# Kernel tuning notes

Hardware: AMD Instinct MI355X
Metric: run time of the kernel (lower is better)

## Reference

```python
import jax, jax.numpy as jnp
import numpy as np

HIDDEN = 1024


def setup_inputs() -> dict:
    key = jax.random.key(0)
    ks = jax.random.split(key, 8)
    x_in, y_in, out_dim, hidden = 1024, 1024, 1024, HIDDEN
    Nx, Ny = 4096, 4096
    s = lambda d: 1.0 / np.sqrt(d)
    return {
        "x": jax.random.normal(ks[0], (Nx, x_in), jnp.float32),
        "y": jax.random.normal(ks[1], (Ny, y_in), jnp.float32),
        "Wq": jax.random.normal(ks[2], (hidden, x_in), jnp.float32) * s(x_in),
        "bq": jnp.zeros((hidden,), jnp.float32),
        "Wk": jax.random.normal(ks[3], (hidden, y_in), jnp.float32) * s(y_in),
        "bk": jnp.zeros((hidden,), jnp.float32),
        "Wv": jax.random.normal(ks[4], (out_dim, y_in), jnp.float32) * s(y_in),
        "bv": jnp.zeros((out_dim,), jnp.float32),
    }


def reference(x, y, Wq, bq, Wk, bk, Wv, bv):
    # Linear projections (torch Linear: x @ W.T + b)
    q = x @ Wq.T + bq          # [Nx, H]
    k = y @ Wk.T + bk          # [Ny, H]
    v = y @ Wv.T + bv          # [Ny, D_out]
    scores = (q @ k.T) / jnp.sqrt(jnp.asarray(HIDDEN, q.dtype))  # [Nx, Ny]
    attn = jax.nn.softmax(scores, axis=1)
    return attn @ v            # [Nx, D_out]
```

## Files before the change

kernel.cpp:

```cpp
#include <hip/hip_runtime.h>
#include <cstdint>
#include <cstddef>

typedef __attribute__((ext_vector_type(8))) __bf16 bf16x8;
typedef __attribute__((ext_vector_type(4))) float  f32x4;

__device__ __forceinline__ unsigned short f32_to_bf16(float f) {
    union { float f; unsigned int u; } cv;
    cv.f = f;
    unsigned int u = cv.u;
    return (unsigned short)((u + 0x7fffu + ((u >> 16) & 1u)) >> 16);
}

__device__ __forceinline__ float bf16_to_f32(unsigned short h) {
    union { unsigned int u; float f; } cv;
    cv.u = ((unsigned int)h) << 16;
    return cv.f;
}

__device__ __forceinline__ void async_copy16(const unsigned short* g, unsigned short* lds) {
    __builtin_amdgcn_global_load_lds(
        (const __attribute__((address_space(1))) unsigned int*)g,
        (__attribute__((address_space(3))) unsigned int*)lds,
        16, 0, 0);
}

__global__ __launch_bounds__(256) void cast_all(
    const float* __restrict__ x,  const float* __restrict__ y,
    const float* __restrict__ wq, const float* __restrict__ wk, const float* __restrict__ wv,
    unsigned short* __restrict__ xb,  unsigned short* __restrict__ yb,
    unsigned short* __restrict__ wqb, unsigned short* __restrict__ wkb,
    unsigned short* __restrict__ wvb, float* __restrict__ lsum)
{
    int b = blockIdx.x;
    if (b >= 11264) {
        float4 z = {0.f, 0.f, 0.f, 0.f};
#pragma unroll
        for (int t = 0; t < 4; ++t)
            ((float4*)lsum)[threadIdx.x * 4 + t] = z;
        return;
    }
    const float* s; unsigned short* d; int base;
    if      (b < 4096)  { s = x;  d = xb;  base = b; }
    else if (b < 8192)  { s = y;  d = yb;  base = b - 4096; }
    else if (b < 9216)  { s = wq; d = wqb; base = b - 8192; }
    else if (b < 10240) { s = wk; d = wkb; base = b - 9216; }
    else                { s = wv; d = wvb; base = b - 10240; }
    int i = base * 256 + threadIdx.x;
    float4 v = ((const float4*)s)[i];
    ushort4 o;
    o.x = f32_to_bf16(v.x);
    o.y = f32_to_bf16(v.y);
    o.z = f32_to_bf16(v.z);
    o.w = f32_to_bf16(v.w);
    ((ushort4*)d)[i] = o;
}

__device__ __forceinline__ void gemm_core_pf(
    const unsigned short* __restrict__ A, const unsigned short* __restrict__ B,
    int K, int rowBase, int colBase, int kBeg, int kEnd,
    unsigned short* ldsA, unsigned short* ldsB, f32x4 acc[4][4])
{
    const int tid  = threadIdx.x;
    const int lane = tid & 63;
    const int wave = tid >> 6;
    const int quad = lane >> 4;
    const int r    = lane & 15;
    const int wm   = wave >> 1;
    const int wn   = wave & 1;

    const int c1 = tid + 256;
    const long aOff0 = (long)(rowBase + (tid >> 2)) * K + (tid & 3) * 8;
    const long aOff1 = (long)(rowBase + (c1  >> 2)) * K + (c1  & 3) * 8;
    const long bOff0 = (long)(colBase + (tid >> 2)) * K + (tid & 3) * 8;
    const long bOff1 = (long)(colBase + (c1  >> 2)) * K + (c1  & 3) * 8;
    unsigned short* ldsA0 = ldsA + tid * 8;
    unsigned short* ldsA1 = ldsA + c1 * 8;
    unsigned short* ldsB0 = ldsB + tid * 8;
    unsigned short* ldsB1 = ldsB + c1 * 8;

    const int aReadOff = (wm * 64 + r) * 32 + quad * 8;
    const int bReadOff = (wn * 64 + r) * 32 + quad * 8;

    const int nSteps = (kEnd - kBeg) >> 5;

    async_copy16(A + aOff0 + kBeg, ldsA0);
    async_copy16(A + aOff1 + kBeg, ldsA1);
    async_copy16(B + bOff0 + kBeg, ldsB0);
    async_copy16(B + bOff1 + kBeg, ldsB1);

    for (int s = 0; s < nSteps; ++s) {
        const int cur = (s & 1) << 12;
        const int nxt = cur ^ 4096;
        __builtin_amdgcn_s_waitcnt(0);
        __syncthreads();
        if (s + 1 < nSteps) {
            const int kn = kBeg + ((s + 1) << 5);
            async_copy16(A + aOff0 + kn, ldsA0 + nxt);
            async_copy16(A + aOff1 + kn, ldsA1 + nxt);
            async_copy16(B + bOff0 + kn, ldsB0 + nxt);
            async_copy16(B + bOff1 + kn, ldsB1 + nxt);
        }
        bf16x8 af[4], bfr[4];
#pragma unroll
        for (int i = 0; i < 4; ++i)
            af[i] = *(const bf16x8*)(ldsA + cur + aReadOff + i * 16 * 32);
#pragma unroll
        for (int j = 0; j < 4; ++j)
            bfr[j] = *(const bf16x8*)(ldsB + cur + bReadOff + j * 16 * 32);
#pragma unroll
        for (int i = 0; i < 4; ++i)
#pragma unroll
            for (int j = 0; j < 4; ++j)
                acc[i][j] = __builtin_amdgcn_mfma_f32_16x16x32_bf16(af[i], bfr[j], acc[i][j], 0, 0, 0);
    }
}

__global__ __launch_bounds__(256, 2)
void proj_batched(const unsigned short* __restrict__ xb, const unsigned short* __restrict__ yb,
                  const unsigned short* __restrict__ wqb, const unsigned short* __restrict__ wkb,
                  const unsigned short* __restrict__ wvb,
                  unsigned short* __restrict__ q, unsigned short* __restrict__ k,
                  unsigned short* __restrict__ vt,
                  const float* __restrict__ bq, const float* __restrict__ bk,
                  const float* __restrict__ bv)
{
    __shared__ __align__(16) unsigned short ldsA[2 * 128 * 32];
    __shared__ __align__(16) unsigned short ldsB[2 * 128 * 32];

    const int b = blockIdx.x;
    const int z = b >> 8;
    const int rb = b & 255;

    const unsigned short *A, *B;
    unsigned short* C;
    const float* bias;
    int N, rowBase, colBase;
    bool biasPerRow;
    if (z == 0) {
        A = xb; B = wqb; C = q; bias = bq; N = 1024; biasPerRow = false;
        colBase = (rb >> 5) * 128; rowBase = (rb & 31) * 128;
    } else if (z == 1) {
        A = yb; B = wkb; C = k; bias = bk; N = 1024; biasPerRow = false;
        colBase = (rb >> 5) * 128; rowBase = (rb & 31) * 128;
    } else {
        A = wvb; B = yb; C = vt; bias = bv; N = 4096; biasPerRow = true;
        colBase = (rb >> 3) * 128; rowBase = (rb & 7) * 128;
    }

    f32x4 acc[4][4];
#pragma unroll
    for (int i = 0; i < 4; ++i)
#pragma unroll
        for (int j = 0; j < 4; ++j)
            acc[i][j] = (f32x4){0.f, 0.f, 0.f, 0.f};

    gemm_core_pf(A, B, 1024, rowBase, colBase, 0, 1024, ldsA, ldsB, acc);

    const int lane = threadIdx.x & 63;
    const int wave = threadIdx.x >> 6;
    const int quad = lane >> 4;
    const int r    = lane & 15;
    const int orow0 = rowBase + (wave >> 1) * 64 + quad * 4;
    const int ocol0 = colBase + (wave & 1) * 64 + r;

#pragma unroll
    for (int i = 0; i < 4; ++i)
#pragma unroll
        for (int e = 0; e < 4; ++e) {
            const int row = orow0 + i * 16 + e;
            const float brow = biasPerRow ? bias[row] : 0.f;
#pragma unroll
            for (int j = 0; j < 4; ++j) {
                const int col = ocol0 + j * 16;
                const float bb = biasPerRow ? brow : bias[col];
                C[(long)row * N + col] = f32_to_bf16(acc[i][j][e] + bb);
            }
        }
}

__global__ __launch_bounds__(256, 2)
void scores_gemm(const unsigned short* __restrict__ q, const unsigned short* __restrict__ k,
                 unsigned short* __restrict__ P, float* __restrict__ lsum, float scale2)
{
    __shared__ __align__(16) unsigned short ldsA[2 * 128 * 32];
    __shared__ __align__(16) unsigned short ldsB[2 * 128 * 32];

    const int rowBase = blockIdx.y * 128;
    const int colBase = blockIdx.x * 128;

    f32x4 acc[4][4];
#pragma unroll
    for (int i = 0; i < 4; ++i)
#pragma unroll
        for (int j = 0; j < 4; ++j)
            acc[i][j] = (f32x4){0.f, 0.f, 0.f, 0.f};

    gemm_core_pf(q, k, 1024, rowBase, colBase, 0, 1024, ldsA, ldsB, acc);

    const int lane = threadIdx.x & 63;
    const int wave = threadIdx.x >> 6;
    const int quad = lane >> 4;
    const int r    = lane & 15;
    const int orow0 = rowBase + (wave >> 1) * 64 + quad * 4;
    const int ocol0 = colBase + (wave & 1) * 64 + r;

#pragma unroll
    for (int i = 0; i < 4; ++i)
#pragma unroll
        for (int e = 0; e < 4; ++e) {
            const int row = orow0 + i * 16 + e;
            float rs = 0.f;
#pragma unroll
            for (int j = 0; j < 4; ++j) {
                const int col = ocol0 + j * 16;
                const float p = exp2f(acc[i][j][e] * scale2);
                rs += p;
                P[(long)row * 4096 + col] = f32_to_bf16(p);
            }
#pragma unroll
            for (int m = 1; m < 16; m <<= 1) rs += __shfl_xor(rs, m, 64);
            if (r == 0) atomicAdd(&lsum[row], rs);
        }
}

template <int ATOMIC>
__global__ __launch_bounds__(256, 2)
void out_gemm_splitk(const unsigned short* __restrict__ P, const unsigned short* __restrict__ vt,
                     void* __restrict__ Out)
{
    __shared__ __align__(16) unsigned short ldsA[2 * 128 * 32];
    __shared__ __align__(16) unsigned short ldsB[2 * 128 * 32];

    const int bid = blockIdx.x;
    const int xt  = bid >> 7;
    const int yz  = bid & 127;
    const int yt  = yz >> 2;
    const int zt  = yz & 3;

    const int rowBase = yt * 128;
    const int colBase = xt * 128;
    const int kBeg = zt * 1024;

    f32x4 acc[4][4];
#pragma unroll
    for (int i = 0; i < 4; ++i)
#pragma unroll
        for (int j = 0; j < 4; ++j)
            acc[i][j] = (f32x4){0.f, 0.f, 0.f, 0.f};

    gemm_core_pf(P, vt, 4096, rowBase, colBase, kBeg, kBeg + 1024, ldsA, ldsB, acc);

    const int lane = threadIdx.x & 63;
    const int wave = threadIdx.x >> 6;
    const int quad = lane >> 4;
    const int r    = lane & 15;
    const int orow0 = rowBase + (wave >> 1) * 64 + quad * 4;
    const int ocol0 = colBase + (wave & 1) * 64 + r;

#pragma unroll
    for (int i = 0; i < 4; ++i)
#pragma unroll
        for (int e = 0; e < 4; ++e) {
            const int row = orow0 + i * 16 + e;
#pragma unroll
            for (int j = 0; j < 4; ++j) {
                const int col = ocol0 + j * 16;
                if (ATOMIC) {
                    atomicAdd(&((float*)Out)[(long)row * 1024 + col], acc[i][j][e]);
                } else {
                    unsigned short* parts = (unsigned short*)Out + (size_t)zt * (4096 * 1024);
                    parts[(long)row * 1024 + col] = f32_to_bf16(acc[i][j][e]);
                }
            }
        }
}

__global__ __launch_bounds__(256) void reduce_norm(const unsigned short* __restrict__ parts,
                                                   const float* __restrict__ lsum,
                                                   float* __restrict__ O) {
    const int i = blockIdx.x * 256 + threadIdx.x;
    const float inv = 1.0f / lsum[i >> 8];
    const size_t stride = (size_t)(4096 * 1024) / 4;
    ushort4 a = ((const ushort4*)parts)[i];
    ushort4 b = ((const ushort4*)parts)[i + stride];
    ushort4 c = ((const ushort4*)parts)[i + 2 * stride];
    ushort4 d = ((const ushort4*)parts)[i + 3 * stride];
    float4 o;
    o.x = (bf16_to_f32(a.x) + bf16_to_f32(b.x) + bf16_to_f32(c.x) + bf16_to_f32(d.x)) * inv;
    o.y = (bf16_to_f32(a.y) + bf16_to_f32(b.y) + bf16_to_f32(c.y) + bf16_to_f32(d.y)) * inv;
    o.z = (bf16_to_f32(a.z) + bf16_to_f32(b.z) + bf16_to_f32(c.z) + bf16_to_f32(d.z)) * inv;
    o.w = (bf16_to_f32(a.w) + bf16_to_f32(b.w) + bf16_to_f32(c.w) + bf16_to_f32(d.w)) * inv;
    ((float4*)O)[i] = o;
}

__global__ __launch_bounds__(256) void norm_rows(float* __restrict__ O, const float* __restrict__ lsum) {
    int i = blockIdx.x * 256 + threadIdx.x;
    const float inv = 1.0f / lsum[i >> 8];
    float4 v = ((const float4*)O)[i];
    v.x *= inv; v.y *= inv; v.z *= inv; v.w *= inv;
    ((float4*)O)[i] = v;
}

extern "C" void kernel_launch(void* const* d_in, const int* in_sizes, int n_in,
                              void* d_out, int out_size, void* d_ws, size_t ws_size,
                              hipStream_t stream) {
    const float* x  = (const float*)d_in[0];
    const float* y  = (const float*)d_in[1];
    const float* Wq = (const float*)d_in[2];
    const float* bq = (const float*)d_in[3];
    const float* Wk = (const float*)d_in[4];
    const float* bk = (const float*)d_in[5];
    const float* Wv = (const float*)d_in[6];
    const float* bv = (const float*)d_in[7];

    constexpr int Nx = 4096, Ny = 4096, H = 1024, Dv = 1024, Kin = 1024;

    char* ws = (char*)d_ws;
    size_t off = 0;
    auto carve = [&](size_t bytes) {
        char* p = ws + off;
        off += (bytes + 255) & ~(size_t)255;
        return p;
    };

    unsigned short* q_bf  = (unsigned short*)carve((size_t)Nx * H * 2);
    unsigned short* k_bf  = (unsigned short*)carve((size_t)Ny * H * 2);
    unsigned short* vt_bf = (unsigned short*)carve((size_t)Dv * Ny * 2);
    float*          lsum  = (float*)carve((size_t)Nx * sizeof(float));

    char* overlay = ws + off;
    unsigned short* x_bf  = (unsigned short*)overlay;
    unsigned short* y_bf  = x_bf  + (size_t)Nx * Kin;
    unsigned short* Wq_bf = y_bf  + (size_t)Ny * Kin;
    unsigned short* Wk_bf = Wq_bf + (size_t)H  * Kin;
    unsigned short* Wv_bf = Wk_bf + (size_t)H  * Kin;
    unsigned short* P_bf  = (unsigned short*)overlay;

    const size_t overlay_bytes = (size_t)Nx * Ny * 2;
    unsigned short* parts = (unsigned short*)(overlay + overlay_bytes);
    const size_t need_parts = (overlay + overlay_bytes + 4 * (size_t)Nx * Dv * 2) - ws;
    const bool useParts = ws_size >= need_parts;

    if (!useParts)
        hipMemsetAsync(d_out, 0, (size_t)Nx * Dv * sizeof(float), stream);

    cast_all<<<11265, 256, 0, stream>>>(x, y, Wq, Wk, Wv, x_bf, y_bf, Wq_bf, Wk_bf, Wv_bf, lsum);

    proj_batched<<<768, 256, 0, stream>>>(x_bf, y_bf, Wq_bf, Wk_bf, Wv_bf,
                                          q_bf, k_bf, vt_bf, bq, bk, bv);

    const float scale2 = 1.4426950408889634f / 32.0f;
    scores_gemm<<<dim3(Ny / 128, Nx / 128), 256, 0, stream>>>(q_bf, k_bf, P_bf, lsum, scale2);

    if (useParts) {
        out_gemm_splitk<0><<<1024, 256, 0, stream>>>(P_bf, vt_bf, parts);
        reduce_norm<<<Nx * Dv / 4 / 256, 256, 0, stream>>>(parts, lsum, (float*)d_out);
    } else {
        out_gemm_splitk<1><<<1024, 256, 0, stream>>>(P_bf, vt_bf, d_out);
        norm_rows<<<Nx * Dv / 4 / 256, 256, 0, stream>>>((float*)d_out, lsum);
    }
}
```

Measured before the change: 240.2 us.

## Fuse all stages into one persistent cooperative kernel with grid syncs

Replaces the chain of separate launches (cast, projections, scores, split-K output GEMM, reduce/normalize) with one cooperative persistent kernel. The kernel loops over tiles for each stage and separates stages with grid-wide barriers. The goal is to remove per-launch overhead and the idle tails between kernels. In exchange the grid is capped by occupancy, which may lower concurrency for the GEMM stages, and grid.sync adds its own cost. The previous multi-kernel path is kept as a fallback if the cooperative launch fails.

Measured after the change: 560.1 us. 133% more time.

```diff
diff --git a/kernel.cpp b/kernel.cpp
--- a/kernel.cpp
+++ b/kernel.cpp
@@ -1,6 +1,9 @@
 #include <hip/hip_runtime.h>
+#include <hip/hip_cooperative_groups.h>
 #include <cstdint>
 #include <cstddef>
+
+namespace cg = cooperative_groups;
 
 typedef __attribute__((ext_vector_type(8))) __bf16 bf16x8;
 typedef __attribute__((ext_vector_type(4))) float  f32x4;
@@ -23,6 +26,264 @@
         (const __attribute__((address_space(1))) unsigned int*)g,
         (__attribute__((address_space(3))) unsigned int*)lds,
         16, 0, 0);
+}
+
+__device__ __forceinline__ void gemm_core_pf(
+    const unsigned short* __restrict__ A, const unsigned short* __restrict__ B,
+    int K, int rowBase, int colBase, int kBeg, int kEnd,
+    unsigned short* ldsA, unsigned short* ldsB, f32x4 acc[4][4])
+{
+    const int tid  = threadIdx.x;
+    const int lane = tid & 63;
+    const int wave = tid >> 6;
+    const int quad = lane >> 4;
+    const int r    = lane & 15;
+    const int wm   = wave >> 1;
+    const int wn   = wave & 1;
+
+    const int c1 = tid + 256;
+    const long aOff0 = (long)(rowBase + (tid >> 2)) * K + (tid & 3) * 8;
+    const long aOff1 = (long)(rowBase + (c1  >> 2)) * K + (c1  & 3) * 8;
+    const long bOff0 = (long)(colBase + (tid >> 2)) * K + (tid & 3) * 8;
+    const long bOff1 = (long)(colBase + (c1  >> 2)) * K + (c1  & 3) * 8;
+    unsigned short* ldsA0 = ldsA + tid * 8;
+    unsigned short* ldsA1 = ldsA + c1 * 8;
+    unsigned short* ldsB0 = ldsB + tid * 8;
+    unsigned short* ldsB1 = ldsB + c1 * 8;
+
+    const int aReadOff = (wm * 64 + r) * 32 + quad * 8;
+    const int bReadOff = (wn * 64 + r) * 32 + quad * 8;
+
+    const int nSteps = (kEnd - kBeg) >> 5;
+
+    async_copy16(A + aOff0 + kBeg, ldsA0);
+    async_copy16(A + aOff1 + kBeg, ldsA1);
+    async_copy16(B + bOff0 + kBeg, ldsB0);
+    async_copy16(B + bOff1 + kBeg, ldsB1);
+
+    for (int s = 0; s < nSteps; ++s) {
+        const int cur = (s & 1) << 12;
+        const int nxt = cur ^ 4096;
+        __builtin_amdgcn_s_waitcnt(0);
+        __syncthreads();
+        if (s + 1 < nSteps) {
+            const int kn = kBeg + ((s + 1) << 5);
+            async_copy16(A + aOff0 + kn, ldsA0 + nxt);
+            async_copy16(A + aOff1 + kn, ldsA1 + nxt);
+            async_copy16(B + bOff0 + kn, ldsB0 + nxt);
+            async_copy16(B + bOff1 + kn, ldsB1 + nxt);
+        }
+        bf16x8 af[4], bfr[4];
+#pragma unroll
+        for (int i = 0; i < 4; ++i)
+            af[i] = *(const bf16x8*)(ldsA + cur + aReadOff + i * 16 * 32);
+#pragma unroll
+        for (int j = 0; j < 4; ++j)
+            bfr[j] = *(const bf16x8*)(ldsB + cur + bReadOff + j * 16 * 32);
+#pragma unroll
+        for (int i = 0; i < 4; ++i)
+#pragma unroll
+            for (int j = 0; j < 4; ++j)
+                acc[i][j] = __builtin_amdgcn_mfma_f32_16x16x32_bf16(af[i], bfr[j], acc[i][j], 0, 0, 0);
+    }
+}
+
+__global__ __launch_bounds__(256, 4)
+void fused_all(const float* __restrict__ x,  const float* __restrict__ y,
+               const float* __restrict__ wq, const float* __restrict__ wk,
+               const float* __restrict__ wv,
+               const float* __restrict__ bq, const float* __restrict__ bk,
+               const float* __restrict__ bv,
+               unsigned short* __restrict__ xb,  unsigned short* __restrict__ yb,
+               unsigned short* __restrict__ wqb, unsigned short* __restrict__ wkb,
+               unsigned short* __restrict__ wvb,
+               unsigned short* __restrict__ qb, unsigned short* __restrict__ kb,
+               unsigned short* __restrict__ vtb,
+               unsigned short* __restrict__ P, unsigned short* __restrict__ parts,
+               float* __restrict__ lsum, float* __restrict__ Out, int useParts)
+{
+    cg::grid_group grid = cg::this_grid();
+    __shared__ __align__(16) unsigned short ldsA[2 * 128 * 32];
+    __shared__ __align__(16) unsigned short ldsB[2 * 128 * 32];
+
+    const int nb   = gridDim.x;
+    const int tid  = threadIdx.x;
+    const int lane = tid & 63;
+    const int wave = tid >> 6;
+    const int quad = lane >> 4;
+    const int r    = lane & 15;
+
+    for (int b = blockIdx.x; b < 11264; b += nb) {
+        const float* s; unsigned short* d; int base;
+        if      (b < 4096)  { s = x;  d = xb;  base = b; }
+        else if (b < 8192)  { s = y;  d = yb;  base = b - 4096; }
+        else if (b < 9216)  { s = wq; d = wqb; base = b - 8192; }
+        else if (b < 10240) { s = wk; d = wkb; base = b - 9216; }
+        else                { s = wv; d = wvb; base = b - 10240; }
+        int i = base * 256 + tid;
+        float4 v = ((const float4*)s)[i];
+        ushort4 o;
+        o.x = f32_to_bf16(v.x);
+        o.y = f32_to_bf16(v.y);
+        o.z = f32_to_bf16(v.z);
+        o.w = f32_to_bf16(v.w);
+        ((ushort4*)d)[i] = o;
+    }
+    if (blockIdx.x == 0) {
+        float4 z = {0.f, 0.f, 0.f, 0.f};
+        for (int t = tid; t < 1024; t += 256) ((float4*)lsum)[t] = z;
+    }
+    if (!useParts) {
+        float4 z = {0.f, 0.f, 0.f, 0.f};
+        for (int i = blockIdx.x * 256 + tid; i < 1024 * 1024; i += nb * 256)
+            ((float4*)Out)[i] = z;
+    }
+    grid.sync();
+
+    for (int t = blockIdx.x; t < 768; t += nb) {
+        const int z = t >> 8;
+        const int rb = t & 255;
+        const unsigned short *A, *B;
+        unsigned short* C;
+        const float* bias;
+        int N, rowBase, colBase;
+        bool biasPerRow;
+        if (z == 0) {
+            A = xb; B = wqb; C = qb; bias = bq; N = 1024; biasPerRow = false;
+            colBase = (rb >> 5) * 128; rowBase = (rb & 31) * 128;
+        } else if (z == 1) {
+            A = yb; B = wkb; C = kb; bias = bk; N = 1024; biasPerRow = false;
+            colBase = (rb >> 5) * 128; rowBase = (rb & 31) * 128;
+        } else {
+            A = wvb; B = yb; C = vtb; bias = bv; N = 4096; biasPerRow = true;
+            colBase = (rb >> 3) * 128; rowBase = (rb & 7) * 128;
+        }
+
+        f32x4 acc[4][4];
+#pragma unroll
+        for (int i = 0; i < 4; ++i)
+#pragma unroll
+            for (int j = 0; j < 4; ++j)
+                acc[i][j] = (f32x4){0.f, 0.f, 0.f, 0.f};
+
+        gemm_core_pf(A, B, 1024, rowBase, colBase, 0, 1024, ldsA, ldsB, acc);
+
+        const int orow0 = rowBase + (wave >> 1) * 64 + quad * 4;
+        const int ocol0 = colBase + (wave & 1) * 64 + r;
+#pragma unroll
+        for (int i = 0; i < 4; ++i)
+#pragma unroll
+            for (int e = 0; e < 4; ++e) {
+                const int row = orow0 + i * 16 + e;
+                const float brow = biasPerRow ? bias[row] : 0.f;
+#pragma unroll
+                for (int j = 0; j < 4; ++j) {
+                    const int col = ocol0 + j * 16;
+                    const float bb = biasPerRow ? brow : bias[col];
+                    C[(long)row * N + col] = f32_to_bf16(acc[i][j][e] + bb);
+                }
+            }
+    }
+    grid.sync();
+
+    const float scale2 = 1.4426950408889634f / 32.0f;
+    for (int t = blockIdx.x; t < 1024; t += nb) {
+        const int rowBase = (t >> 5) * 128;
+        const int colBase = (t & 31) * 128;
+
+        f32x4 acc[4][4];
+#pragma unroll
+        for (int i = 0; i < 4; ++i)
+#pragma unroll
+            for (int j = 0; j < 4; ++j)
+                acc[i][j] = (f32x4){0.f, 0.f, 0.f, 0.f};
+
+        gemm_core_pf(qb, kb, 1024, rowBase, colBase, 0, 1024, ldsA, ldsB, acc);
+
+        const int orow0 = rowBase + (wave >> 1) * 64 + quad * 4;
+        const int ocol0 = colBase + (wave & 1) * 64 + r;
+#pragma unroll
+        for (int i = 0; i < 4; ++i)
+#pragma unroll
+            for (int e = 0; e < 4; ++e) {
+                const int row = orow0 + i * 16 + e;
+                float rs = 0.f;
+#pragma unroll
+                for (int j = 0; j < 4; ++j) {
+                    const int col = ocol0 + j * 16;
+                    const float p = exp2f(acc[i][j][e] * scale2);
+                    rs += p;
+                    P[(long)row * 4096 + col] = f32_to_bf16(p);
+                }
+#pragma unroll
+                for (int m = 1; m < 16; m <<= 1) rs += __shfl_xor(rs, m, 64);
+                if (r == 0) atomicAdd(&lsum[row], rs);
+            }
+    }
+    grid.sync();
+
+    for (int t = blockIdx.x; t < 1024; t += nb) {
+        const int xt = t >> 7;
+        const int yz = t & 127;
+        const int yt = yz >> 2;
+        const int zt = yz & 3;
+        const int rowBase = yt * 128;
+        const int colBase = xt * 128;
+        const int kBeg = zt * 1024;
+
+        f32x4 acc[4][4];
+#pragma unroll
+        for (int i = 0; i < 4; ++i)
+#pragma unroll
+            for (int j = 0; j < 4; ++j)
+                acc[i][j] = (f32x4){0.f, 0.f, 0.f, 0.f};
+
+        gemm_core_pf(P, vtb, 4096, rowBase, colBase, kBeg, kBeg + 1024, ldsA, ldsB, acc);
+
+        const int orow0 = rowBase + (wave >> 1) * 64 + quad * 4;
+        const int ocol0 = colBase + (wave & 1) * 64 + r;
+#pragma unroll
+        for (int i = 0; i < 4; ++i)
+#pragma unroll
+            for (int e = 0; e < 4; ++e) {
+                const int row = orow0 + i * 16 + e;
+#pragma unroll
+                for (int j = 0; j < 4; ++j) {
+                    const int col = ocol0 + j * 16;
+                    if (useParts) {
+                        unsigned short* pz = parts + (size_t)zt * (4096 * 1024);
+                        pz[(long)row * 1024 + col] = f32_to_bf16(acc[i][j][e]);
+                    } else {
+                        atomicAdd(&Out[(long)row * 1024 + col], acc[i][j][e]);
+                    }
+                }
+            }
+    }
+    grid.sync();
+
+    if (useParts) {
+        const size_t stride = (size_t)(4096 * 1024) / 4;
+        for (int i = blockIdx.x * 256 + tid; i < 1024 * 1024; i += nb * 256) {
+            const float inv = 1.0f / lsum[i >> 8];
+            ushort4 a = ((const ushort4*)parts)[i];
+            ushort4 b = ((const ushort4*)parts)[i + stride];
+            ushort4 c = ((const ushort4*)parts)[i + 2 * stride];
+            ushort4 d = ((const ushort4*)parts)[i + 3 * stride];
+            float4 o;
+            o.x = (bf16_to_f32(a.x) + bf16_to_f32(b.x) + bf16_to_f32(c.x) + bf16_to_f32(d.x)) * inv;
+            o.y = (bf16_to_f32(a.y) + bf16_to_f32(b.y) + bf16_to_f32(c.y) + bf16_to_f32(d.y)) * inv;
+            o.z = (bf16_to_f32(a.z) + bf16_to_f32(b.z) + bf16_to_f32(c.z) + bf16_to_f32(d.z)) * inv;
+            o.w = (bf16_to_f32(a.w) + bf16_to_f32(b.w) + bf16_to_f32(c.w) + bf16_to_f32(d.w)) * inv;
+            ((float4*)Out)[i] = o;
+        }
+    } else {
+        for (int i = blockIdx.x * 256 + tid; i < 1024 * 1024; i += nb * 256) {
+            const float inv = 1.0f / lsum[i >> 8];
+            float4 v = ((const float4*)Out)[i];
+            v.x *= inv; v.y *= inv; v.z *= inv; v.w *= inv;
+            ((float4*)Out)[i] = v;
+        }
+    }
 }
 
 __global__ __launch_bounds__(256) void cast_all(
@@ -54,66 +315,6 @@
     o.z = f32_to_bf16(v.z);
     o.w = f32_to_bf16(v.w);
     ((ushort4*)d)[i] = o;
-}
-
-__device__ __forceinline__ void gemm_core_pf(
-    const unsigned short* __restrict__ A, const unsigned short* __restrict__ B,
-    int K, int rowBase, int colBase, int kBeg, int kEnd,
-    unsigned short* ldsA, unsigned short* ldsB, f32x4 acc[4][4])
-{
-    const int tid  = threadIdx.x;
-    const int lane = tid & 63;
-    const int wave = tid >> 6;
-    const int quad = lane >> 4;
-    const int r    = lane & 15;
-    const int wm   = wave >> 1;
-    const int wn   = wave & 1;
-
-    const int c1 = tid + 256;
-    const long aOff0 = (long)(rowBase + (tid >> 2)) * K + (tid & 3) * 8;
-    const long aOff1 = (long)(rowBase + (c1  >> 2)) * K + (c1  & 3) * 8;
-    const long bOff0 = (long)(colBase + (tid >> 2)) * K + (tid & 3) * 8;
-    const long bOff1 = (long)(colBase + (c1  >> 2)) * K + (c1  & 3) * 8;
-    unsigned short* ldsA0 = ldsA + tid * 8;
-    unsigned short* ldsA1 = ldsA + c1 * 8;
-    unsigned short* ldsB0 = ldsB + tid * 8;
-    unsigned short* ldsB1 = ldsB + c1 * 8;
-
-    const int aReadOff = (wm * 64 + r) * 32 + quad * 8;
-    const int bReadOff = (wn * 64 + r) * 32 + quad * 8;
-
-    const int nSteps = (kEnd - kBeg) >> 5;
-
-    async_copy16(A + aOff0 + kBeg, ldsA0);
-    async_copy16(A + aOff1 + kBeg, ldsA1);
-    async_copy16(B + bOff0 + kBeg, ldsB0);
-    async_copy16(B + bOff1 + kBeg, ldsB1);
-
-    for (int s = 0; s < nSteps; ++s) {
-        const int cur = (s & 1) << 12;
-        const int nxt = cur ^ 4096;
-        __builtin_amdgcn_s_waitcnt(0);
-        __syncthreads();
-        if (s + 1 < nSteps) {
-            const int kn = kBeg + ((s + 1) << 5);
-            async_copy16(A + aOff0 + kn, ldsA0 + nxt);
-            async_copy16(A + aOff1 + kn, ldsA1 + nxt);
-            async_copy16(B + bOff0 + kn, ldsB0 + nxt);
-            async_copy16(B + bOff1 + kn, ldsB1 + nxt);
-        }
-        bf16x8 af[4], bfr[4];
-#pragma unroll
-        for (int i = 0; i < 4; ++i)
-            af[i] = *(const bf16x8*)(ldsA + cur + aReadOff + i * 16 * 32);
-#pragma unroll
-        for (int j = 0; j < 4; ++j)
-            bfr[j] = *(const bf16x8*)(ldsB + cur + bReadOff + j * 16 * 32);
-#pragma unroll
-        for (int i = 0; i < 4; ++i)
-#pragma unroll
-            for (int j = 0; j < 4; ++j)
-                acc[i][j] = __builtin_amdgcn_mfma_f32_16x16x32_bf16(af[i], bfr[j], acc[i][j], 0, 0, 0);
-    }
 }
 
 __global__ __launch_bounds__(256, 2)
@@ -340,24 +541,39 @@
     const size_t overlay_bytes = (size_t)Nx * Ny * 2;
     unsigned short* parts = (unsigned short*)(overlay + overlay_bytes);
     const size_t need_parts = (overlay + overlay_bytes + 4 * (size_t)Nx * Dv * 2) - ws;
-    const bool useParts = ws_size >= need_parts;
-
-    if (!useParts)
-        hipMemsetAsync(d_out, 0, (size_t)Nx * Dv * sizeof(float), stream);
-
-    cast_all<<<11265, 256, 0, stream>>>(x, y, Wq, Wk, Wv, x_bf, y_bf, Wq_bf, Wk_bf, Wv_bf, lsum);
-
-    proj_batched<<<768, 256, 0, stream>>>(x_bf, y_bf, Wq_bf, Wk_bf, Wv_bf,
-                                          q_bf, k_bf, vt_bf, bq, bk, bv);
-
-    const float scale2 = 1.4426950408889634f / 32.0f;
-    scores_gemm<<<dim3(Ny / 128, Nx / 128), 256, 0, stream>>>(q_bf, k_bf, P_bf, lsum, scale2);
-
-    if (useParts) {
-        out_gemm_splitk<0><<<1024, 256, 0, stream>>>(P_bf, vt_bf, parts);
-        reduce_norm<<<Nx * Dv / 4 / 256, 256, 0, stream>>>(parts, lsum, (float*)d_out);
-    } else {
-        out_gemm_splitk<1><<<1024, 256, 0, stream>>>(P_bf, vt_bf, d_out);
-        norm_rows<<<Nx * Dv / 4 / 256, 256, 0, stream>>>((float*)d_out, lsum);
-    }
-}
+    int useParts = (ws_size >= need_parts) ? 1 : 0;
+    float* Out = (float*)d_out;
+
+    int blocksPerCU = 0;
+    hipError_t qerr = hipOccupancyMaxActiveBlocksPerMultiprocessor(
+        &blocksPerCU, (const void*)fused_all, 256, 0);
+    if (qerr != hipSuccess || blocksPerCU < 1) blocksPerCU = 2;
+    if (blocksPerCU > 4) blocksPerCU = 4;
+    int nblocks = 256 * blocksPerCU;
+    if (nblocks > 1024) nblocks = 1024;
+
+    void* args[] = { &x, &y, &Wq, &Wk, &Wv, &bq, &bk, &bv,
+                     &x_bf, &y_bf, &Wq_bf, &Wk_bf, &Wv_bf,
+                     &q_bf, &k_bf, &vt_bf,
+                     &P_bf, &parts, &lsum, &Out, &useParts };
+
+    hipError_t lerr = hipLaunchCooperativeKernel(
+        (const void*)fused_all, dim3(nblocks), dim3(256), args, 0, stream);
+
+    if (lerr != hipSuccess) {
+        if (!useParts)
+            hipMemsetAsync(d_out, 0, (size_t)Nx * Dv * sizeof(float), stream);
+        cast_all<<<11265, 256, 0, stream>>>(x, y, Wq, Wk, Wv, x_bf, y_bf, Wq_bf, Wk_bf, Wv_bf, lsum);
+        proj_batched<<<768, 256, 0, stream>>>(x_bf, y_bf, Wq_bf, Wk_bf, Wv_bf,
+                                              q_bf, k_bf, vt_bf, bq, bk, bv);
+        const float scale2 = 1.4426950408889634f / 32.0f;
+        scores_gemm<<<dim3(Ny / 128, Nx / 128), 256, 0, stream>>>(q_bf, k_bf, P_bf, lsum, scale2);
+        if (useParts) {
+            out_gemm_splitk<0><<<1024, 256, 0, stream>>>(P_bf, vt_bf, parts);
+            reduce_norm<<<Nx * Dv / 4 / 256, 256, 0, stream>>>(parts, lsum, (float*)d_out);
+        } else {
+            out_gemm_splitk<1><<<1024, 256, 0, stream>>>(P_bf, vt_bf, d_out);
+            norm_rows<<<Nx * Dv / 4 / 256, 256, 0, stream>>>((float*)d_out, lsum);
+        }
+    }
+}
```

## Fuse split-K reduction and row normalization into output GEMM via last-block counter

Applied to the files above, without the earlier changes.

Removes the separate reduce_norm kernel. Each split-K block writes its bf16 partial and then increments a per-tile counter, and the last of the four blocks sums the partials, applies the softmax row normalization and writes the fp32 output. This saves one kernel launch and lets the reduction overlap with other tiles' GEMM work. In exchange it adds threadfences and atomics, makes the reduction serial inside the last block of each tile, and needs the counters zeroed in cast_all.

Result: slower. 487.6 us (+103.0%).

```diff
diff --git a/kernel.cpp b/kernel.cpp
--- a/kernel.cpp
+++ b/kernel.cpp
@@ -30,7 +30,7 @@
     const float* __restrict__ wq, const float* __restrict__ wk, const float* __restrict__ wv,
     unsigned short* __restrict__ xb,  unsigned short* __restrict__ yb,
     unsigned short* __restrict__ wqb, unsigned short* __restrict__ wkb,
-    unsigned short* __restrict__ wvb, float* __restrict__ lsum)
+    unsigned short* __restrict__ wvb, float* __restrict__ lsum, int* __restrict__ cnt)
 {
     int b = blockIdx.x;
     if (b >= 11264) {
@@ -38,6 +38,7 @@
 #pragma unroll
         for (int t = 0; t < 4; ++t)
             ((float4*)lsum)[threadIdx.x * 4 + t] = z;
+        if (threadIdx.x < 64) ((int4*)cnt)[threadIdx.x] = (int4){0, 0, 0, 0};
         return;
     }
     const float* s; unsigned short* d; int base;
@@ -227,7 +228,8 @@
 template <int ATOMIC>
 __global__ __launch_bounds__(256, 2)
 void out_gemm_splitk(const unsigned short* __restrict__ P, const unsigned short* __restrict__ vt,
-                     void* __restrict__ Out)
+                     unsigned short* __restrict__ parts, int* __restrict__ cnt,
+                     const float* __restrict__ lsum, float* __restrict__ Out)
 {
     __shared__ __align__(16) unsigned short ldsA[2 * 128 * 32];
     __shared__ __align__(16) unsigned short ldsB[2 * 128 * 32];
@@ -258,40 +260,53 @@
     const int orow0 = rowBase + (wave >> 1) * 64 + quad * 4;
     const int ocol0 = colBase + (wave & 1) * 64 + r;
 
+    if (ATOMIC) {
+#pragma unroll
+        for (int i = 0; i < 4; ++i)
+#pragma unroll
+            for (int e = 0; e < 4; ++e) {
+                const int row = orow0 + i * 16 + e;
+#pragma unroll
+                for (int j = 0; j < 4; ++j)
+                    atomicAdd(&Out[(long)row * 1024 + ocol0 + j * 16], acc[i][j][e]);
+            }
+        return;
+    }
+
+    unsigned short* pz = parts + (size_t)zt * (4096 * 1024);
 #pragma unroll
     for (int i = 0; i < 4; ++i)
 #pragma unroll
         for (int e = 0; e < 4; ++e) {
             const int row = orow0 + i * 16 + e;
 #pragma unroll
-            for (int j = 0; j < 4; ++j) {
-                const int col = ocol0 + j * 16;
-                if (ATOMIC) {
-                    atomicAdd(&((float*)Out)[(long)row * 1024 + col], acc[i][j][e]);
-                } else {
-                    unsigned short* parts = (unsigned short*)Out + (size_t)zt * (4096 * 1024);
-                    parts[(long)row * 1024 + col] = f32_to_bf16(acc[i][j][e]);
-                }
-            }
-        }
-}
-
-__global__ __launch_bounds__(256) void reduce_norm(const unsigned short* __restrict__ parts,
-                                                   const float* __restrict__ lsum,
-                                                   float* __restrict__ O) {
-    const int i = blockIdx.x * 256 + threadIdx.x;
-    const float inv = 1.0f / lsum[i >> 8];
-    const size_t stride = (size_t)(4096 * 1024) / 4;
-    ushort4 a = ((const ushort4*)parts)[i];
-    ushort4 b = ((const ushort4*)parts)[i + stride];
-    ushort4 c = ((const ushort4*)parts)[i + 2 * stride];
-    ushort4 d = ((const ushort4*)parts)[i + 3 * stride];
-    float4 o;
-    o.x = (bf16_to_f32(a.x) + bf16_to_f32(b.x) + bf16_to_f32(c.x) + bf16_to_f32(d.x)) * inv;
-    o.y = (bf16_to_f32(a.y) + bf16_to_f32(b.y) + bf16_to_f32(c.y) + bf16_to_f32(d.y)) * inv;
-    o.z = (bf16_to_f32(a.z) + bf16_to_f32(b.z) + bf16_to_f32(c.z) + bf16_to_f32(d.z)) * inv;
-    o.w = (bf16_to_f32(a.w) + bf16_to_f32(b.w) + bf16_to_f32(c.w) + bf16_to_f32(d.w)) * inv;
-    ((float4*)O)[i] = o;
+            for (int j = 0; j < 4; ++j)
+                pz[(long)row * 1024 + ocol0 + j * 16] = f32_to_bf16(acc[i][j][e]);
+        }
+
+    __threadfence();
+    __shared__ int lastFlag;
+    if (threadIdx.x == 0)
+        lastFlag = atomicAdd(&cnt[yt * 8 + xt], 1);
+    __syncthreads();
+    if (lastFlag != 3) return;
+    __threadfence();
+
+    const size_t zs = (size_t)4096 * 1024;
+    for (int it = threadIdx.x; it < 4096; it += 256) {
+        const int row = rowBase + (it >> 5);
+        const size_t base = (size_t)row * 1024 + colBase + ((it & 31) << 2);
+        const float inv = 1.0f / lsum[row];
+        float s0 = 0.f, s1 = 0.f, s2 = 0.f, s3 = 0.f;
+#pragma unroll
+        for (int z = 0; z < 4; ++z) {
+            ushort4 a = *(const ushort4*)(parts + z * zs + base);
+            s0 += bf16_to_f32(a.x); s1 += bf16_to_f32(a.y);
+            s2 += bf16_to_f32(a.z); s3 += bf16_to_f32(a.w);
+        }
+        float4 o = {s0 * inv, s1 * inv, s2 * inv, s3 * inv};
+        *(float4*)(&Out[base]) = o;
+    }
 }
 
 __global__ __launch_bounds__(256) void norm_rows(float* __restrict__ O, const float* __restrict__ lsum) {
@@ -328,6 +343,7 @@
     unsigned short* k_bf  = (unsigned short*)carve((size_t)Ny * H * 2);
     unsigned short* vt_bf = (unsigned short*)carve((size_t)Dv * Ny * 2);
     float*          lsum  = (float*)carve((size_t)Nx * sizeof(float));
+    int*            cnt   = (int*)carve(256 * sizeof(int));
 
     char* overlay = ws + off;
     unsigned short* x_bf  = (unsigned short*)overlay;
@@ -345,7 +361,8 @@
     if (!useParts)
         hipMemsetAsync(d_out, 0, (size_t)Nx * Dv * sizeof(float), stream);
 
-    cast_all<<<11265, 256, 0, stream>>>(x, y, Wq, Wk, Wv, x_bf, y_bf, Wq_bf, Wk_bf, Wv_bf, lsum);
+    cast_all<<<11265, 256, 0, stream>>>(x, y, Wq, Wk, Wv, x_bf, y_bf, Wq_bf, Wk_bf, Wv_bf,
+                                        lsum, cnt);
 
     proj_batched<<<768, 256, 0, stream>>>(x_bf, y_bf, Wq_bf, Wk_bf, Wv_bf,
                                           q_bf, k_bf, vt_bf, bq, bk, bv);
@@ -354,10 +371,9 @@
     scores_gemm<<<dim3(Ny / 128, Nx / 128), 256, 0, stream>>>(q_bf, k_bf, P_bf, lsum, scale2);
 
     if (useParts) {
-        out_gemm_splitk<0><<<1024, 256, 0, stream>>>(P_bf, vt_bf, parts);
-        reduce_norm<<<Nx * Dv / 4 / 256, 256, 0, stream>>>(parts, lsum, (float*)d_out);
+        out_gemm_splitk<0><<<1024, 256, 0, stream>>>(P_bf, vt_bf, parts, cnt, lsum, (float*)d_out);
     } else {
-        out_gemm_splitk<1><<<1024, 256, 0, stream>>>(P_bf, vt_bf, d_out);
+        out_gemm_splitk<1><<<1024, 256, 0, stream>>>(P_bf, vt_bf, nullptr, cnt, lsum, (float*)d_out);
         norm_rows<<<Nx * Dv / 4 / 256, 256, 0, stream>>>((float*)d_out, lsum);
     }
 }
```

## Fuse fp32-to-bf16 cast into projection GEMM, dropping separate cast kernel

Applied to the files above, without the earlier changes.

Removes the standalone cast kernel and has the projection GEMM load fp32 inputs directly. The loaded values are converted to bf16 in registers, stored to LDS, and the next tile is prefetched through registers. The lsum zeroing moves into block 0 of the projection kernel. This saves the bf16 write-back and re-read of x, y and the weights plus one launch. In exchange, each GEMM block reads fp32 data from global memory, twice the bytes of bf16, and the cast work is repeated for every tile that reuses the same inputs. It also loses the async global-to-LDS copy path.

Result: no change. 243.4 us (+1.3%).

```diff
diff --git a/kernel.cpp b/kernel.cpp
--- a/kernel.cpp
+++ b/kernel.cpp
@@ -23,37 +23,6 @@
         (const __attribute__((address_space(1))) unsigned int*)g,
         (__attribute__((address_space(3))) unsigned int*)lds,
         16, 0, 0);
-}
-
-__global__ __launch_bounds__(256) void cast_all(
-    const float* __restrict__ x,  const float* __restrict__ y,
-    const float* __restrict__ wq, const float* __restrict__ wk, const float* __restrict__ wv,
-    unsigned short* __restrict__ xb,  unsigned short* __restrict__ yb,
-    unsigned short* __restrict__ wqb, unsigned short* __restrict__ wkb,
-    unsigned short* __restrict__ wvb, float* __restrict__ lsum)
-{
-    int b = blockIdx.x;
-    if (b >= 11264) {
-        float4 z = {0.f, 0.f, 0.f, 0.f};
-#pragma unroll
-        for (int t = 0; t < 4; ++t)
-            ((float4*)lsum)[threadIdx.x * 4 + t] = z;
-        return;
-    }
-    const float* s; unsigned short* d; int base;
-    if      (b < 4096)  { s = x;  d = xb;  base = b; }
-    else if (b < 8192)  { s = y;  d = yb;  base = b - 4096; }
-    else if (b < 9216)  { s = wq; d = wqb; base = b - 8192; }
-    else if (b < 10240) { s = wk; d = wkb; base = b - 9216; }
-    else                { s = wv; d = wvb; base = b - 10240; }
-    int i = base * 256 + threadIdx.x;
-    float4 v = ((const float4*)s)[i];
-    ushort4 o;
-    o.x = f32_to_bf16(v.x);
-    o.y = f32_to_bf16(v.y);
-    o.z = f32_to_bf16(v.z);
-    o.w = f32_to_bf16(v.w);
-    ((ushort4*)d)[i] = o;
 }
 
 __device__ __forceinline__ void gemm_core_pf(
@@ -117,34 +86,43 @@
 }
 
 __global__ __launch_bounds__(256, 2)
-void proj_batched(const unsigned short* __restrict__ xb, const unsigned short* __restrict__ yb,
-                  const unsigned short* __restrict__ wqb, const unsigned short* __restrict__ wkb,
-                  const unsigned short* __restrict__ wvb,
-                  unsigned short* __restrict__ q, unsigned short* __restrict__ k,
-                  unsigned short* __restrict__ vt,
-                  const float* __restrict__ bq, const float* __restrict__ bk,
-                  const float* __restrict__ bv)
+void proj_batched_f32(const float* __restrict__ x, const float* __restrict__ y,
+                      const float* __restrict__ wq, const float* __restrict__ wk,
+                      const float* __restrict__ wv,
+                      unsigned short* __restrict__ q, unsigned short* __restrict__ k,
+                      unsigned short* __restrict__ vt,
+                      const float* __restrict__ bq, const float* __restrict__ bk,
+                      const float* __restrict__ bv, float* __restrict__ lsum)
 {
     __shared__ __align__(16) unsigned short ldsA[2 * 128 * 32];
     __shared__ __align__(16) unsigned short ldsB[2 * 128 * 32];
 
     const int b = blockIdx.x;
+    const int tid = threadIdx.x;
+
+    if (b == 0) {
+        float4 zz = {0.f, 0.f, 0.f, 0.f};
+#pragma unroll
+        for (int t = 0; t < 4; ++t)
+            ((float4*)lsum)[tid * 4 + t] = zz;
+    }
+
     const int z = b >> 8;
     const int rb = b & 255;
 
-    const unsigned short *A, *B;
+    const float *A, *B;
     unsigned short* C;
     const float* bias;
     int N, rowBase, colBase;
     bool biasPerRow;
     if (z == 0) {
-        A = xb; B = wqb; C = q; bias = bq; N = 1024; biasPerRow = false;
+        A = x; B = wq; C = q; bias = bq; N = 1024; biasPerRow = false;
         colBase = (rb >> 5) * 128; rowBase = (rb & 31) * 128;
     } else if (z == 1) {
-        A = yb; B = wkb; C = k; bias = bk; N = 1024; biasPerRow = false;
+        A = y; B = wk; C = k; bias = bk; N = 1024; biasPerRow = false;
         colBase = (rb >> 5) * 128; rowBase = (rb & 31) * 128;
     } else {
-        A = wvb; B = yb; C = vt; bias = bv; N = 4096; biasPerRow = true;
+        A = wv; B = y; C = vt; bias = bv; N = 4096; biasPerRow = true;
         colBase = (rb >> 3) * 128; rowBase = (rb & 7) * 128;
     }
 
@@ -155,12 +133,63 @@
         for (int j = 0; j < 4; ++j)
             acc[i][j] = (f32x4){0.f, 0.f, 0.f, 0.f};
 
-    gemm_core_pf(A, B, 1024, rowBase, colBase, 0, 1024, ldsA, ldsB, acc);
-
-    const int lane = threadIdx.x & 63;
-    const int wave = threadIdx.x >> 6;
+    const int lane = tid & 63;
+    const int wave = tid >> 6;
     const int quad = lane >> 4;
     const int r    = lane & 15;
+    const int aReadOff = ((wave >> 1) * 64 + r) * 32 + quad * 8;
+    const int bReadOff = ((wave & 1) * 64 + r) * 32 + quad * 8;
+
+    long gA[4], gB[4];
+#pragma unroll
+    for (int i = 0; i < 4; ++i) {
+        const int f = tid + 256 * i;
+        gA[i] = (long)(rowBase + (f >> 3)) * 256 + (f & 7);
+        gB[i] = (long)(colBase + (f >> 3)) * 256 + (f & 7);
+    }
+
+    float4 ra[4], rbv[4];
+#pragma unroll
+    for (int i = 0; i < 4; ++i) {
+        ra[i]  = ((const float4*)A)[gA[i]];
+        rbv[i] = ((const float4*)B)[gB[i]];
+    }
+
+    for (int s = 0; s < 32; ++s) {
+        const int buf = (s & 1) << 12;
+#pragma unroll
+        for (int i = 0; i < 4; ++i) {
+            ushort4 ua, ub;
+            ua.x = f32_to_bf16(ra[i].x);  ua.y = f32_to_bf16(ra[i].y);
+            ua.z = f32_to_bf16(ra[i].z);  ua.w = f32_to_bf16(ra[i].w);
+            ub.x = f32_to_bf16(rbv[i].x); ub.y = f32_to_bf16(rbv[i].y);
+            ub.z = f32_to_bf16(rbv[i].z); ub.w = f32_to_bf16(rbv[i].w);
+            ((ushort4*)(ldsA + buf))[tid + 256 * i] = ua;
+            ((ushort4*)(ldsB + buf))[tid + 256 * i] = ub;
+        }
+        __syncthreads();
+        if (s + 1 < 32) {
+            const int kt8 = (s + 1) * 8;
+#pragma unroll
+            for (int i = 0; i < 4; ++i) {
+                ra[i]  = ((const float4*)A)[gA[i] + kt8];
+                rbv[i] = ((const float4*)B)[gB[i] + kt8];
+            }
+        }
+        bf16x8 af[4], bfr[4];
+#pragma unroll
+        for (int i = 0; i < 4; ++i)
+            af[i] = *(const bf16x8*)(ldsA + buf + aReadOff + i * 16 * 32);
+#pragma unroll
+        for (int j = 0; j < 4; ++j)
+            bfr[j] = *(const bf16x8*)(ldsB + buf + bReadOff + j * 16 * 32);
+#pragma unroll
+        for (int i = 0; i < 4; ++i)
+#pragma unroll
+            for (int j = 0; j < 4; ++j)
+                acc[i][j] = __builtin_amdgcn_mfma_f32_16x16x32_bf16(af[i], bfr[j], acc[i][j], 0, 0, 0);
+    }
+
     const int orow0 = rowBase + (wave >> 1) * 64 + quad * 4;
     const int ocol0 = colBase + (wave & 1) * 64 + r;
 
@@ -329,26 +358,16 @@
     unsigned short* vt_bf = (unsigned short*)carve((size_t)Dv * Ny * 2);
     float*          lsum  = (float*)carve((size_t)Nx * sizeof(float));
 
-    char* overlay = ws + off;
-    unsigned short* x_bf  = (unsigned short*)overlay;
-    unsigned short* y_bf  = x_bf  + (size_t)Nx * Kin;
-    unsigned short* Wq_bf = y_bf  + (size_t)Ny * Kin;
-    unsigned short* Wk_bf = Wq_bf + (size_t)H  * Kin;
-    unsigned short* Wv_bf = Wk_bf + (size_t)H  * Kin;
-    unsigned short* P_bf  = (unsigned short*)overlay;
-
-    const size_t overlay_bytes = (size_t)Nx * Ny * 2;
-    unsigned short* parts = (unsigned short*)(overlay + overlay_bytes);
-    const size_t need_parts = (overlay + overlay_bytes + 4 * (size_t)Nx * Dv * 2) - ws;
+    unsigned short* P_bf  = (unsigned short*)carve((size_t)Nx * Ny * 2);
+    unsigned short* parts = (unsigned short*)(ws + off);
+    const size_t need_parts = off + 4 * (size_t)Nx * Dv * 2;
     const bool useParts = ws_size >= need_parts;
 
     if (!useParts)
         hipMemsetAsync(d_out, 0, (size_t)Nx * Dv * sizeof(float), stream);
 
-    cast_all<<<11265, 256, 0, stream>>>(x, y, Wq, Wk, Wv, x_bf, y_bf, Wq_bf, Wk_bf, Wv_bf, lsum);
-
-    proj_batched<<<768, 256, 0, stream>>>(x_bf, y_bf, Wq_bf, Wk_bf, Wv_bf,
-                                          q_bf, k_bf, vt_bf, bq, bk, bv);
+    proj_batched_f32<<<768, 256, 0, stream>>>(x, y, Wq, Wk, Wv,
+                                              q_bf, k_bf, vt_bf, bq, bk, bv, lsum);
 
     const float scale2 = 1.4426950408889634f / 32.0f;
     scores_gemm<<<dim3(Ny / 128, Nx / 128), 256, 0, stream>>>(q_bf, k_bf, P_bf, lsum, scale2);
```
